# Kernel optimization log

Hardware: AMD Instinct MI355X
Metric: run time of the kernel (lower is better)

The kernel has to match this reference:

```python
import jax, jax.numpy as jnp
import numpy as np

BN_EPS = 1e-5


def setup_inputs() -> dict:
    key = jax.random.key(0)
    ks = jax.random.split(key, 8)
    B, C, H, W = 8, 256, 64, 64
    Ci = 128
    s_in = 1.0 / np.sqrt(C)
    s_int = 1.0 / np.sqrt(Ci)
    return {
        "x": jax.random.normal(ks[0], (B, C, H, W), jnp.float32),
        "w_g": jax.random.normal(ks[1], (Ci, C), jnp.float32) * s_in,
        "b_g": jnp.zeros((Ci,), jnp.float32),
        "w_theta": jax.random.normal(ks[2], (Ci, C), jnp.float32) * s_in,
        "b_theta": jnp.zeros((Ci,), jnp.float32),
        "w_phi": jax.random.normal(ks[3], (Ci, C), jnp.float32) * s_in,
        "b_phi": jnp.zeros((Ci,), jnp.float32),
        "w_out": jax.random.normal(ks[4], (C, Ci), jnp.float32) * s_int,
        "b_out": jnp.zeros((C,), jnp.float32),
        "bn_gamma": jnp.ones((C,), jnp.float32),
        "bn_beta": jnp.zeros((C,), jnp.float32),
        "bn_mean": jnp.zeros((C,), jnp.float32),
        "bn_var": jnp.ones((C,), jnp.float32),
    }


def reference(x, w_g, b_g, w_theta, b_theta, w_phi, b_phi, w_out, b_out,
              bn_gamma, bn_beta, bn_mean, bn_var):
    B, C, H, W = x.shape
    Ci = w_g.shape[0]
    N = H * W
    # 1x1 convs == per-pixel linear projections
    g = (jnp.einsum('bchw,oc->bhwo', x, w_g) + b_g).reshape(B, N, Ci)
    theta = (jnp.einsum('bchw,oc->bhwo', x, w_theta) + b_theta).reshape(B, N, Ci)
    phi = (jnp.einsum('bchw,oc->bohw', x, w_phi) + b_phi[:, None, None]).reshape(B, Ci, N)
    # full N x N attention (no scaling, as in the original)
    att = jax.nn.softmax(jnp.einsum('bnc,bcm->bnm', theta, phi), axis=-1)
    y = jnp.einsum('bnm,bmc->bnc', att, g).reshape(B, H, W, Ci)
    # output 1x1 conv + inference-mode BatchNorm (per-channel affine)
    out = jnp.einsum('bhwc,oc->bohw', y, w_out) + b_out[:, None, None]
    inv = bn_gamma / jnp.sqrt(bn_var + BN_EPS)
    out = out * inv[:, None, None] + (bn_beta - bn_mean * inv)[:, None, None]
    return x + out
```

## Files before the change

kernel.cpp:

```cpp
#include <hip/hip_runtime.h>
#include <math.h>

#define BB 8
#define CC 256
#define CI 128
#define NN 4096
#define BN_EPS 1e-5f
#define LOG2E 1.4426950408889634f
#define FIXMAX 88.0f

typedef unsigned int uint;
typedef unsigned short ushort;
typedef __bf16 bf16x8 __attribute__((ext_vector_type(8)));
typedef _Float16 f16x8 __attribute__((ext_vector_type(8)));
typedef float f32x16 __attribute__((ext_vector_type(16)));

__device__ __forceinline__ ushort bfbits(float f) {
    return __builtin_bit_cast(ushort, (__bf16)f);
}
__device__ __forceinline__ ushort hbits(float f) {
    return __builtin_bit_cast(ushort, (_Float16)f);
}
__device__ __forceinline__ float bf2f(ushort h) {
    return __uint_as_float(((uint)h) << 16);
}
__device__ __forceinline__ uint pk2(float a, float b) {
    return (uint)bfbits(a) | ((uint)bfbits(b) << 16);
}
__device__ __forceinline__ void gload16(const void* g, void* l) {
    __builtin_amdgcn_global_load_lds(
        (const __attribute__((address_space(1))) uint*)g,
        (__attribute__((address_space(3))) uint*)l, 16, 0, 0);
}
__device__ __forceinline__ bf16x8 asbf8(uint4 v) { return __builtin_bit_cast(bf16x8, v); }
__device__ __forceinline__ float fexp2(float a) {
    float e;
    asm("v_exp_f32 %0, %1" : "=v"(e) : "v"(a));
    return e;
}

__global__ __launch_bounds__(256) void wconv_kernel(
    const float* __restrict__ w_t, const float* __restrict__ w_p,
    const float* __restrict__ w_g, const float* __restrict__ w_o,
    const float* __restrict__ bn_g, const float* __restrict__ bn_b,
    const float* __restrict__ bn_m, const float* __restrict__ bn_v,
    const float* __restrict__ b_out,
    uint4* __restrict__ wt_h, uint4* __restrict__ wt_l,
    uint4* __restrict__ wp_h, uint4* __restrict__ wp_l,
    uint4* __restrict__ wg_h, uint4* __restrict__ wg_l,
    uint4* __restrict__ wo_h, uint4* __restrict__ wo_l,
    float* __restrict__ scale, float* __restrict__ shift)
{
    const int t = threadIdx.x, blk = blockIdx.x;
    if (blk == 64) {
        float inv = bn_g[t] * rsqrtf(bn_v[t] + BN_EPS);
        scale[t] = inv;
        shift[t] = b_out[t] * inv + bn_b[t] - bn_m[t] * inv;
        return;
    }
    int u = blk * 256 + t;
    int mat = u >> 12, ul = u & 4095;
    const float* src;
    uint4 *dh, *dl;
    int o, oct, C, O;
    if (mat == 0)      { src = w_t; dh = wt_h; dl = wt_l; }
    else if (mat == 1) { src = w_p; dh = wp_h; dl = wp_l; }
    else if (mat == 2) { src = w_g; dh = wg_h; dl = wg_l; }
    else               { src = w_o; dh = wo_h; dl = wo_l; }
    if (mat < 3) { O = 128; C = 256; o = ul >> 5; oct = ul & 31; }
    else         { O = 256; C = 128; o = ul >> 4; oct = ul & 15; }
    const float* s = src + (size_t)o * C + oct * 8;
    float4 va = *(const float4*)s, vb = *(const float4*)(s + 4);
    float v[8] = {va.x, va.y, va.z, va.w, vb.x, vb.y, vb.z, vb.w};
    uint hw[4], lw[4];
#pragma unroll
    for (int j = 0; j < 4; j++) {
        float a = v[2 * j], c = v[2 * j + 1];
        ushort ha = bfbits(a), hc = bfbits(c);
        hw[j] = (uint)ha | ((uint)hc << 16);
        lw[j] = pk2(a - bf2f(ha), c - bf2f(hc));
    }
    int di = oct * O + o;
    dh[di] = make_uint4(hw[0], hw[1], hw[2], hw[3]);
    dl[di] = make_uint4(lw[0], lw[1], lw[2], lw[3]);
}

__global__ __launch_bounds__(256, 2) void proj3_mfma(
    const float* __restrict__ x,
    const uint4* __restrict__ wt_h, const uint4* __restrict__ wt_l,
    const uint4* __restrict__ wp_h, const uint4* __restrict__ wp_l,
    const uint4* __restrict__ wg_h, const uint4* __restrict__ wg_l,
    const float* __restrict__ b_t, const float* __restrict__ b_p,
    const float* __restrict__ b_g,
    ushort* __restrict__ th, ushort* __restrict__ phi, ushort* __restrict__ gT)
{
    __shared__ __align__(16) char xsm[65536];
    const int t  = threadIdx.x;
    const int w  = t >> 6, l = t & 63;
    const int lq = l & 31, h = l >> 5;
    const int b  = blockIdx.x >> 6;
    const int n0 = (blockIdx.x & 63) << 6;

    {
        const int nq = t & 15;
#pragma unroll
        for (int i = 0; i < 2; i++) {
            int oct = (t >> 4) + 16 * i;
            const float* xp = x + ((size_t)b * CC + oct * 8) * NN + n0 + nq * 4;
            float4 r[8];
#pragma unroll
            for (int j = 0; j < 8; j++) r[j] = *(const float4*)(xp + (size_t)j * NN);
#pragma unroll
            for (int k = 0; k < 4; k++) {
                int n = nq * 4 + k;
                float v[8];
#pragma unroll
                for (int j = 0; j < 8; j++) v[j] = ((const float*)&r[j])[k];
                uint hw[4], lw[4];
#pragma unroll
                for (int j = 0; j < 4; j++) {
                    ushort ha = bfbits(v[2 * j]), hc = bfbits(v[2 * j + 1]);
                    hw[j] = (uint)ha | ((uint)hc << 16);
                    lw[j] = pk2(v[2 * j] - bf2f(ha), v[2 * j + 1] - bf2f(hc));
                }
                int uu = oct ^ (n & 31);
                *(uint4*)(xsm + n * 512 + uu * 16) = make_uint4(hw[0], hw[1], hw[2], hw[3]);
                *(uint4*)(xsm + 32768 + n * 512 + uu * 16) = make_uint4(lw[0], lw[1], lw[2], lw[3]);
            }
        }
    }
    __syncthreads();

    const int wo16 = w * 32 + lq;
    f32x16 acc[3][2];
    {
        float bt = b_t[wo16], bp = b_p[wo16];
        acc[0][0] = (f32x16)bt; acc[0][1] = (f32x16)bt;
        acc[1][0] = (f32x16)bp; acc[1][1] = (f32x16)bp;
        acc[2][0] = (f32x16)0.0f; acc[2][1] = (f32x16)0.0f;
    }

#pragma unroll 2
    for (int cs = 0; cs < 16; cs++) {
        int wi = (cs * 2 + h) * 128 + wo16;
        bf16x8 fth = asbf8(wt_h[wi]), ftl = asbf8(wt_l[wi]);
        bf16x8 fph = asbf8(wp_h[wi]), fpl = asbf8(wp_l[wi]);
        bf16x8 fgh = asbf8(wg_h[wi]), fgl = asbf8(wg_l[wi]);
        int xoff = lq * 512 + 16 * ((cs * 2 + h) ^ lq);
        bf16x8 xh0 = asbf8(*(const uint4*)(xsm + xoff));
        bf16x8 xh1 = asbf8(*(const uint4*)(xsm + 16384 + xoff));
        bf16x8 xl0 = asbf8(*(const uint4*)(xsm + 32768 + xoff));
        bf16x8 xl1 = asbf8(*(const uint4*)(xsm + 49152 + xoff));

        acc[0][0] = __builtin_amdgcn_mfma_f32_32x32x16_bf16(xh0, fth, acc[0][0], 0, 0, 0);
        acc[0][0] = __builtin_amdgcn_mfma_f32_32x32x16_bf16(xl0, fth, acc[0][0], 0, 0, 0);
        acc[0][0] = __builtin_amdgcn_mfma_f32_32x32x16_bf16(xh0, ftl, acc[0][0], 0, 0, 0);
        acc[0][1] = __builtin_amdgcn_mfma_f32_32x32x16_bf16(xh1, fth, acc[0][1], 0, 0, 0);
        acc[0][1] = __builtin_amdgcn_mfma_f32_32x32x16_bf16(xl1, fth, acc[0][1], 0, 0, 0);
        acc[0][1] = __builtin_amdgcn_mfma_f32_32x32x16_bf16(xh1, ftl, acc[0][1], 0, 0, 0);

        acc[1][0] = __builtin_amdgcn_mfma_f32_32x32x16_bf16(xh0, fph, acc[1][0], 0, 0, 0);
        acc[1][0] = __builtin_amdgcn_mfma_f32_32x32x16_bf16(xl0, fph, acc[1][0], 0, 0, 0);
        acc[1][0] = __builtin_amdgcn_mfma_f32_32x32x16_bf16(xh0, fpl, acc[1][0], 0, 0, 0);
        acc[1][1] = __builtin_amdgcn_mfma_f32_32x32x16_bf16(xh1, fph, acc[1][1], 0, 0, 0);
        acc[1][1] = __builtin_amdgcn_mfma_f32_32x32x16_bf16(xl1, fph, acc[1][1], 0, 0, 0);
        acc[1][1] = __builtin_amdgcn_mfma_f32_32x32x16_bf16(xh1, fpl, acc[1][1], 0, 0, 0);

        acc[2][0] = __builtin_amdgcn_mfma_f32_32x32x16_bf16(fgh, xh0, acc[2][0], 0, 0, 0);
        acc[2][0] = __builtin_amdgcn_mfma_f32_32x32x16_bf16(fgh, xl0, acc[2][0], 0, 0, 0);
        acc[2][0] = __builtin_amdgcn_mfma_f32_32x32x16_bf16(fgl, xh0, acc[2][0], 0, 0, 0);
        acc[2][1] = __builtin_amdgcn_mfma_f32_32x32x16_bf16(fgh, xh1, acc[2][1], 0, 0, 0);
        acc[2][1] = __builtin_amdgcn_mfma_f32_32x32x16_bf16(fgh, xl1, acc[2][1], 0, 0, 0);
        acc[2][1] = __builtin_amdgcn_mfma_f32_32x32x16_bf16(fgl, xh1, acc[2][1], 0, 0, 0);
    }

#pragma unroll
    for (int ns = 0; ns < 2; ns++) {
        size_t nb = (size_t)b * NN + n0 + ns * 32;
#pragma unroll
        for (int r = 0; r < 16; r++) {
            int nr = (r & 3) + 8 * (r >> 2) + 4 * h;
            size_t idx = (nb + nr) * CI + wo16;
            th[idx]  = hbits(acc[0][ns][r] * LOG2E);
            phi[idx] = hbits(acc[1][ns][r]);
        }
#pragma unroll
        for (int r = 0; r < 16; r++) {
            int orow = w * 32 + (r & 3) + 8 * (r >> 2) + 4 * h;
            gT[((size_t)b * CI + orow) * NN + n0 + ns * 32 + lq] =
                bfbits(acc[2][ns][r] + b_g[orow]);
        }
    }
}

__global__ __launch_bounds__(512, 2) void attn_mfma(
    const ushort* __restrict__ th, const ushort* __restrict__ phi,
    const ushort* __restrict__ gT,
    ushort* __restrict__ yh, ushort* __restrict__ yl)
{
    __shared__ __align__(16) char sm[131072];
    const int t    = threadIdx.x;
    const int w    = t >> 6, l = t & 63;
    const int wg   = w & 3, half = w >> 2;
    const int lq   = l & 31, h = l >> 5;
    const int b    = blockIdx.x & 7, qt = blockIdx.x >> 3;
    const int q0   = qt * 128 + wg * 32;

    f16x8 thf[8];
    {
        const char* thp = (const char*)(th + ((size_t)b * NN + q0 + lq) * CI);
#pragma unroll
        for (int cs = 0; cs < 8; cs++)
            thf[cs] = __builtin_bit_cast(f16x8, *(const uint4*)(thp + cs * 32 + h * 16));
    }

    const char* phig = (const char*)(phi + (size_t)b * NN * CI);
    const char* gTg  = (const char*)(gT + (size_t)b * NN * CI);
    char* smh = sm + half * 65536;

    f32x16 ya[4];
#pragma unroll
    for (int ct = 0; ct < 4; ct++) ya[ct] = (f32x16)0.0f;
    float l_run = 0.0f;

    auto stage = [&](int buf, int tile) {
        const char* ps = phig + (size_t)tile * 16384;
        const char* gs = gTg + (size_t)tile * 128;
        char* lb = smh + buf * 32768;
#pragma unroll
        for (int j = 0; j < 4; j++) {
            int c  = wg * 4 + j;
            int r  = c * 4 + (l >> 4);
            int cp = ((l & 15) * 16) ^ ((r & 15) << 4);
            gload16(ps + (size_t)r * 256 + cp, lb + c * 1024);
            int r8 = c * 8 + (l >> 3);
            int cg = ((l & 7) * 16) ^ ((r8 & 7) << 4);
            gload16(gs + (size_t)r8 * (NN * 2) + cg, lb + 16384 + c * 1024);
        }
    };

    stage(0, half * 32 + 0);
    stage(1, half * 32 + 1);
    asm volatile("s_waitcnt vmcnt(8)" ::: "memory");
    __builtin_amdgcn_s_barrier();
    __builtin_amdgcn_sched_barrier(0);

    const int swp = (lq & 15) << 4;
    const int swg = (lq & 7) << 4;

    for (int it = 0; it < 32; it++) {
        const char* smb = smh + (it & 1) * 32768;

        f32x16 sa0 = (f32x16)0.0f, sa1 = (f32x16)0.0f;
        __builtin_amdgcn_s_setprio(1);
#pragma unroll
        for (int cs = 0; cs < 8; cs++) {
            f16x8 f0 = __builtin_bit_cast(f16x8,
                *(const uint4*)(smb + lq * 256 + ((cs * 32 + h * 16) ^ swp)));
            f16x8 f1 = __builtin_bit_cast(f16x8,
                *(const uint4*)(smb + (32 + lq) * 256 + ((cs * 32 + h * 16) ^ swp)));
            sa0 = __builtin_amdgcn_mfma_f32_32x32x16_f16(f0, thf[cs], sa0, 0, 0, 0);
            sa1 = __builtin_amdgcn_mfma_f32_32x32x16_f16(f1, thf[cs], sa1, 0, 0, 0);
        }
        __builtin_amdgcn_s_setprio(0);

        {
            float t0 = 0.f, t1 = 0.f, t2 = 0.f, t3 = 0.f;
#pragma unroll
            for (int r = 0; r < 16; r += 4) {
                sa0[r]     = fexp2(sa0[r] - FIXMAX);     t0 += sa0[r];
                sa0[r + 1] = fexp2(sa0[r + 1] - FIXMAX); t1 += sa0[r + 1];
                sa0[r + 2] = fexp2(sa0[r + 2] - FIXMAX); t2 += sa0[r + 2];
                sa0[r + 3] = fexp2(sa0[r + 3] - FIXMAX); t3 += sa0[r + 3];
            }
#pragma unroll
            for (int r = 0; r < 16; r += 4) {
                sa1[r]     = fexp2(sa1[r] - FIXMAX);     t0 += sa1[r];
                sa1[r + 1] = fexp2(sa1[r + 1] - FIXMAX); t1 += sa1[r + 1];
                sa1[r + 2] = fexp2(sa1[r + 2] - FIXMAX); t2 += sa1[r + 2];
                sa1[r + 3] = fexp2(sa1[r + 3] - FIXMAX); t3 += sa1[r + 3];
            }
            l_run += (t0 + t1) + (t2 + t3);
        }

        __builtin_amdgcn_s_setprio(1);
#pragma unroll
        for (int mt = 0; mt < 2; mt++) {
            const f32x16& pa = mt ? sa1 : sa0;
#pragma unroll
            for (int s = 0; s < 2; s++) {
                const int base = s * 8;
                uint a0 = pk2(pa[base + 0], pa[base + 1]);
                uint a1 = pk2(pa[base + 2], pa[base + 3]);
                uint b0 = pk2(pa[base + 4], pa[base + 5]);
                uint b1 = pk2(pa[base + 6], pa[base + 7]);
                asm volatile("v_permlane32_swap_b32 %0, %1" : "+v"(a0), "+v"(b0));
                asm volatile("v_permlane32_swap_b32 %0, %1" : "+v"(a1), "+v"(b1));
                bf16x8 pf = __builtin_bit_cast(bf16x8, make_uint4(a0, a1, b0, b1));
                const int ks = mt * 2 + s;
#pragma unroll
                for (int ct = 0; ct < 4; ct++) {
                    bf16x8 gf = __builtin_bit_cast(bf16x8,
                        *(const uint4*)(smb + 16384 + (ct * 32 + lq) * 128 +
                                        ((ks * 32 + h * 16) ^ swg)));
                    ya[ct] = __builtin_amdgcn_mfma_f32_32x32x16_bf16(gf, pf, ya[ct], 0, 0, 0);
                }
            }
        }
        __builtin_amdgcn_s_setprio(0);

        asm volatile("" ::: "memory");
        __builtin_amdgcn_s_barrier();
        if (it < 30) {
            stage(it & 1, half * 32 + it + 2);
            asm volatile("s_waitcnt vmcnt(8)" ::: "memory");
            __builtin_amdgcn_s_barrier();
            __builtin_amdgcn_sched_barrier(0);
        } else if (it == 30) {
            asm volatile("s_waitcnt vmcnt(0)" ::: "memory");
            __builtin_amdgcn_s_barrier();
            __builtin_amdgcn_sched_barrier(0);
        }
    }

    if (w >= 4) {
        float* dst = (float*)(sm + wg * 16384 + l * 256);
#pragma unroll
        for (int ct = 0; ct < 4; ct++)
#pragma unroll
            for (int r4 = 0; r4 < 4; r4++) {
                int u = (ct * 4 + r4) ^ (l & 15);
                *(float4*)((char*)dst + u * 16) =
                    make_float4(ya[ct][r4 * 4 + 0], ya[ct][r4 * 4 + 1],
                                ya[ct][r4 * 4 + 2], ya[ct][r4 * 4 + 3]);
            }
        ((float*)(sm + 65536))[wg * 64 + l] = l_run;
    }
    __syncthreads();
    if (w < 4) {
        float lself = l_run + __shfl_xor(l_run, 32);
        const float* lBp = (const float*)(sm + 65536) + wg * 64;
        float ltot = lself + lBp[lq] + lBp[lq + 32];
        float inv = 1.0f / ltot;
        const char* src = (const char*)(sm + wg * 16384 + l * 256);
        const size_t qb = ((size_t)b * NN + q0 + lq) * CI;
#pragma unroll
        for (int ct = 0; ct < 4; ct++)
#pragma unroll
            for (int r4 = 0; r4 < 4; r4++) {
                int u = (ct * 4 + r4) ^ (l & 15);
                float4 vB = *(const float4*)(src + u * 16);
                float v0 = (ya[ct][r4 * 4 + 0] + vB.x) * inv;
                float v1 = (ya[ct][r4 * 4 + 1] + vB.y) * inv;
                float v2 = (ya[ct][r4 * 4 + 2] + vB.z) * inv;
                float v3 = (ya[ct][r4 * 4 + 3] + vB.w) * inv;
                ushort h0 = bfbits(v0), h1 = bfbits(v1), h2 = bfbits(v2), h3 = bfbits(v3);
                uint2 hw = make_uint2((uint)h0 | ((uint)h1 << 16),
                                      (uint)h2 | ((uint)h3 << 16));
                uint2 lw = make_uint2(pk2(v0 - bf2f(h0), v1 - bf2f(h1)),
                                      pk2(v2 - bf2f(h2), v3 - bf2f(h3)));
                int co = 32 * ct + 8 * r4 + 4 * h;
                *(uint2*)(yh + qb + co) = hw;
                *(uint2*)(yl + qb + co) = lw;
            }
    }
}

__global__ __launch_bounds__(256, 2) void outproj_mfma(
    const ushort* __restrict__ yh, const ushort* __restrict__ yl,
    const uint4* __restrict__ wo_h, const uint4* __restrict__ wo_l,
    const float* __restrict__ scale, const float* __restrict__ shift,
    const float* __restrict__ x, float* __restrict__ out)
{
    __shared__ __align__(16) char ysm[32768];
    const int t  = threadIdx.x;
    const int w  = t >> 6, l = t & 63;
    const int lq = l & 31, h = l >> 5;
    const int b  = blockIdx.x >> 6;
    const int n0 = (blockIdx.x & 63) << 6;

    {
#pragma unroll
        for (int j = 0; j < 4; j++) {
            int idx = w * 64 + j * 256 + l;
            int row = idx >> 4, u = idx & 15;
            size_t srow = ((size_t)b * NN + n0 + row) * CI;
            int cb = 16 * (u ^ (row & 15));
            gload16((const char*)yh + srow * 2 + cb, ysm + (w * 64 + j * 256) * 16);
            gload16((const char*)yl + srow * 2 + cb, ysm + 16384 + (w * 64 + j * 256) * 16);
        }
    }
    __syncthreads();

#pragma unroll
    for (int oi = 0; oi < 2; oi++) {
        const int ot = w + oi * 4;
        const int ob = ot * 32 + lq;
        f32x16 a0 = (f32x16)0.0f, a1 = (f32x16)0.0f;
#pragma unroll 2
        for (int cs = 0; cs < 8; cs++) {
            int wi = (cs * 2 + h) * 256 + ob;
            bf16x8 wfh = asbf8(wo_h[wi]), wfl = asbf8(wo_l[wi]);
            int xoff = lq * 256 + 16 * ((cs * 2 + h) ^ (lq & 15));
            bf16x8 y0h = asbf8(*(const uint4*)(ysm + xoff));
            bf16x8 y1h = asbf8(*(const uint4*)(ysm + 8192 + xoff));
            bf16x8 y0l = asbf8(*(const uint4*)(ysm + 16384 + xoff));
            bf16x8 y1l = asbf8(*(const uint4*)(ysm + 24576 + xoff));
            a0 = __builtin_amdgcn_mfma_f32_32x32x16_bf16(wfh, y0h, a0, 0, 0, 0);
            a0 = __builtin_amdgcn_mfma_f32_32x32x16_bf16(wfl, y0h, a0, 0, 0, 0);
            a0 = __builtin_amdgcn_mfma_f32_32x32x16_bf16(wfh, y0l, a0, 0, 0, 0);
            a1 = __builtin_amdgcn_mfma_f32_32x32x16_bf16(wfh, y1h, a1, 0, 0, 0);
            a1 = __builtin_amdgcn_mfma_f32_32x32x16_bf16(wfl, y1h, a1, 0, 0, 0);
            a1 = __builtin_amdgcn_mfma_f32_32x32x16_bf16(wfh, y1l, a1, 0, 0, 0);
        }
#pragma unroll
        for (int ns = 0; ns < 2; ns++) {
            const f32x16& av = ns ? a1 : a0;
#pragma unroll
            for (int r = 0; r < 16; r++) {
                int o = ot * 32 + (r & 3) + 8 * (r >> 2) + 4 * h;
                size_t ai = ((size_t)b * CC + o) * NN + n0 + ns * 32 + lq;
                out[ai] = av[r] * scale[o] + shift[o] + x[ai];
            }
        }
    }
}

extern "C" void kernel_launch(void* const* d_in, const int* in_sizes, int n_in,
                              void* d_out, int out_size, void* d_ws, size_t ws_size,
                              hipStream_t stream) {
    const float* x       = (const float*)d_in[0];
    const float* w_g     = (const float*)d_in[1];
    const float* b_g     = (const float*)d_in[2];
    const float* w_theta = (const float*)d_in[3];
    const float* b_theta = (const float*)d_in[4];
    const float* w_phi   = (const float*)d_in[5];
    const float* b_phi   = (const float*)d_in[6];
    const float* w_out   = (const float*)d_in[7];
    const float* b_out   = (const float*)d_in[8];
    const float* bn_g    = (const float*)d_in[9];
    const float* bn_b    = (const float*)d_in[10];
    const float* bn_m    = (const float*)d_in[11];
    const float* bn_v    = (const float*)d_in[12];
    float* out = (float*)d_out;

    const size_t arr = (size_t)BB * NN * CI;
    ushort* thw   = (ushort*)d_ws;
    ushort* phiw  = thw + arr;
    ushort* gTw   = phiw + arr;
    ushort* yhb   = gTw + arr;
    ushort* ylb   = yhb + arr;
    uint4*  wt_h  = (uint4*)(ylb + arr);
    uint4*  wt_l  = wt_h + 4096;
    uint4*  wp_h  = wt_l + 4096;
    uint4*  wp_l  = wp_h + 4096;
    uint4*  wg_h  = wp_l + 4096;
    uint4*  wg_l  = wg_h + 4096;
    uint4*  wo_h  = wg_l + 4096;
    uint4*  wo_l  = wo_h + 4096;
    float*  scl   = (float*)(wo_l + 4096);
    float*  shf   = scl + 256;

    wconv_kernel<<<65, 256, 0, stream>>>(
        w_theta, w_phi, w_g, w_out, bn_g, bn_b, bn_m, bn_v, b_out,
        wt_h, wt_l, wp_h, wp_l, wg_h, wg_l, wo_h, wo_l, scl, shf);
    proj3_mfma<<<BB * 64, 256, 0, stream>>>(
        x, wt_h, wt_l, wp_h, wp_l, wg_h, wg_l, b_theta, b_phi, b_g,
        thw, phiw, gTw);
    attn_mfma<<<256, 512, 0, stream>>>(thw, phiw, gTw, yhb, ylb);
    outproj_mfma<<<BB * 64, 256, 0, stream>>>(
        yhb, ylb, wo_h, wo_l, scl, shf, x, out);
}
```

Measured before the change: 140.7 us.

## Software-pipeline QK^T of the next tile with softmax and PV of the current tile

Splits staging into separate phi and gT double buffers. The QK^T MFMAs for tile it+1 are now issued before the exp/sum and PV work of tile it, so the VALU exponentials can overlap the matrix-core work. Wait counts are adjusted so each phi tile is resident one iteration earlier than its gT tile. This costs an extra pair of 16-wide accumulators per lane, which raises register pressure and could lower occupancy.

```diff
diff --git a/kernel.cpp b/kernel.cpp
--- a/kernel.cpp
+++ b/kernel.cpp
@@ -223,87 +223,105 @@
     for (int ct = 0; ct < 4; ct++) ya[ct] = (f32x16)0.0f;
     float l_run = 0.0f;
 
-    auto stage = [&](int buf, int tile) {
+    auto stage_phi = [&](int slot, int tile) {
         const char* ps = phig + (size_t)tile * 16384;
-        const char* gs = gTg + (size_t)tile * 128;
-        char* lb = smh + buf * 32768;
+        char* lb = smh + slot * 16384;
 #pragma unroll
         for (int j = 0; j < 4; j++) {
             int c  = wg * 4 + j;
             int r  = c * 4 + (l >> 4);
             int cp = ((l & 15) * 16) ^ ((r & 15) << 4);
             gload16(ps + (size_t)r * 256 + cp, lb + c * 1024);
+        }
+    };
+    auto stage_gt = [&](int slot, int tile) {
+        const char* gs = gTg + (size_t)tile * 128;
+        char* lb = smh + 32768 + slot * 16384;
+#pragma unroll
+        for (int j = 0; j < 4; j++) {
+            int c  = wg * 4 + j;
             int r8 = c * 8 + (l >> 3);
             int cg = ((l & 7) * 16) ^ ((r8 & 7) << 4);
-            gload16(gs + (size_t)r8 * (NN * 2) + cg, lb + 16384 + c * 1024);
+            gload16(gs + (size_t)r8 * (NN * 2) + cg, lb + c * 1024);
         }
     };
 
-    stage(0, half * 32 + 0);
-    stage(1, half * 32 + 1);
-    asm volatile("s_waitcnt vmcnt(8)" ::: "memory");
+    const int swp = (lq & 15) << 4;
+    const int swg = (lq & 7) << 4;
+
+    auto qk = [&](const char* pb, f32x16& d0, f32x16& d1) {
+#pragma unroll
+        for (int cs = 0; cs < 8; cs++) {
+            f16x8 f0 = __builtin_bit_cast(f16x8,
+                *(const uint4*)(pb + lq * 256 + ((cs * 32 + h * 16) ^ swp)));
+            f16x8 f1 = __builtin_bit_cast(f16x8,
+                *(const uint4*)(pb + (32 + lq) * 256 + ((cs * 32 + h * 16) ^ swp)));
+            d0 = __builtin_amdgcn_mfma_f32_32x32x16_f16(f0, thf[cs], d0, 0, 0, 0);
+            d1 = __builtin_amdgcn_mfma_f32_32x32x16_f16(f1, thf[cs], d1, 0, 0, 0);
+        }
+    };
+
+    const int t0 = half * 32;
+    stage_phi(0, t0 + 0);
+    stage_phi(1, t0 + 1);
+    stage_gt(0, t0 + 0);
+    stage_gt(1, t0 + 1);
+    asm volatile("s_waitcnt vmcnt(4)" ::: "memory");
     __builtin_amdgcn_s_barrier();
     __builtin_amdgcn_sched_barrier(0);
 
-    const int swp = (lq & 15) << 4;
-    const int swg = (lq & 7) << 4;
+    f32x16 sa0 = (f32x16)0.0f, sa1 = (f32x16)0.0f;
+    __builtin_amdgcn_s_setprio(1);
+    qk(smh, sa0, sa1);
+    __builtin_amdgcn_s_setprio(0);
 
     for (int it = 0; it < 32; it++) {
-        const char* smb = smh + (it & 1) * 32768;
-
-        f32x16 sa0 = (f32x16)0.0f, sa1 = (f32x16)0.0f;
+        f32x16 nx0 = (f32x16)0.0f, nx1 = (f32x16)0.0f;
         __builtin_amdgcn_s_setprio(1);
-#pragma unroll
-        for (int cs = 0; cs < 8; cs++) {
-            f16x8 f0 = __builtin_bit_cast(f16x8,
-                *(const uint4*)(smb + lq * 256 + ((cs * 32 + h * 16) ^ swp)));
-            f16x8 f1 = __builtin_bit_cast(f16x8,
-                *(const uint4*)(smb + (32 + lq) * 256 + ((cs * 32 + h * 16) ^ swp)));
-            sa0 = __builtin_amdgcn_mfma_f32_32x32x16_f16(f0, thf[cs], sa0, 0, 0, 0);
-            sa1 = __builtin_amdgcn_mfma_f32_32x32x16_f16(f1, thf[cs], sa1, 0, 0, 0);
-        }
-        __builtin_amdgcn_s_setprio(0);
+        if (it < 31) qk(smh + ((it + 1) & 1) * 16384, nx0, nx1);
 
         {
-            float t0 = 0.f, t1 = 0.f, t2 = 0.f, t3 = 0.f;
+            float t0s = 0.f, t1s = 0.f, t2s = 0.f, t3s = 0.f;
 #pragma unroll
             for (int r = 0; r < 16; r += 4) {
-                sa0[r]     = fexp2(sa0[r] - FIXMAX);     t0 += sa0[r];
-                sa0[r + 1] = fexp2(sa0[r + 1] - FIXMAX); t1 += sa0[r + 1];
-                sa0[r + 2] = fexp2(sa0[r + 2] - FIXMAX); t2 += sa0[r + 2];
-                sa0[r + 3] = fexp2(sa0[r + 3] - FIXMAX); t3 += sa0[r + 3];
+                sa0[r]     = fexp2(sa0[r] - FIXMAX);     t0s += sa0[r];
+                sa0[r + 1] = fexp2(sa0[r + 1] - FIXMAX); t1s += sa0[r + 1];
+                sa0[r + 2] = fexp2(sa0[r + 2] - FIXMAX); t2s += sa0[r + 2];
+                sa0[r + 3] = fexp2(sa0[r + 3] - FIXMAX); t3s += sa0[r + 3];
             }
 #pragma unroll
             for (int r = 0; r < 16; r += 4) {
-                sa1[r]     = fexp2(sa1[r] - FIXMAX);     t0 += sa1[r];
-                sa1[r + 1] = fexp2(sa1[r + 1] - FIXMAX); t1 += sa1[r + 1];
-                sa1[r + 2] = fexp2(sa1[r + 2] - FIXMAX); t2 += sa1[r + 2];
-                sa1[r + 3] = fexp2(sa1[r + 3] - FIXMAX); t3 += sa1[r + 3];
-            }
-            l_run += (t0 + t1) + (t2 + t3);
-        }
-
-        __builtin_amdgcn_s_setprio(1);
-#pragma unroll
-        for (int mt = 0; mt < 2; mt++) {
-            const f32x16& pa = mt ? sa1 : sa0;
-#pragma unroll
-            for (int s = 0; s < 2; s++) {
-                const int base = s * 8;
-                uint a0 = pk2(pa[base + 0], pa[base + 1]);
-                uint a1 = pk2(pa[base + 2], pa[base + 3]);
-                uint b0 = pk2(pa[base + 4], pa[base + 5]);
-                uint b1 = pk2(pa[base + 6], pa[base + 7]);
-                asm volatile("v_permlane32_swap_b32 %0, %1" : "+v"(a0), "+v"(b0));
-                asm volatile("v_permlane32_swap_b32 %0, %1" : "+v"(a1), "+v"(b1));
-                bf16x8 pf = __builtin_bit_cast(bf16x8, make_uint4(a0, a1, b0, b1));
-                const int ks = mt * 2 + s;
-#pragma unroll
-                for (int ct = 0; ct < 4; ct++) {
-                    bf16x8 gf = __builtin_bit_cast(bf16x8,
-                        *(const uint4*)(smb + 16384 + (ct * 32 + lq) * 128 +
-                                        ((ks * 32 + h * 16) ^ swg)));
-                    ya[ct] = __builtin_amdgcn_mfma_f32_32x32x16_bf16(gf, pf, ya[ct], 0, 0, 0);
+                sa1[r]     = fexp2(sa1[r] - FIXMAX);     t0s += sa1[r];
+                sa1[r + 1] = fexp2(sa1[r + 1] - FIXMAX); t1s += sa1[r + 1];
+                sa1[r + 2] = fexp2(sa1[r + 2] - FIXMAX); t2s += sa1[r + 2];
+                sa1[r + 3] = fexp2(sa1[r + 3] - FIXMAX); t3s += sa1[r + 3];
+            }
+            l_run += (t0s + t1s) + (t2s + t3s);
+        }
+
+        {
+            const char* gb = smh + 32768 + (it & 1) * 16384;
+#pragma unroll
+            for (int mt = 0; mt < 2; mt++) {
+                const f32x16& pa = mt ? sa1 : sa0;
+#pragma unroll
+                for (int s = 0; s < 2; s++) {
+                    const int base = s * 8;
+                    uint a0 = pk2(pa[base + 0], pa[base + 1]);
+                    uint a1 = pk2(pa[base + 2], pa[base + 3]);
+                    uint b0 = pk2(pa[base + 4], pa[base + 5]);
+                    uint b1 = pk2(pa[base + 6], pa[base + 7]);
+                    asm volatile("v_permlane32_swap_b32 %0, %1" : "+v"(a0), "+v"(b0));
+                    asm volatile("v_permlane32_swap_b32 %0, %1" : "+v"(a1), "+v"(b1));
+                    bf16x8 pf = __builtin_bit_cast(bf16x8, make_uint4(a0, a1, b0, b1));
+                    const int ks = mt * 2 + s;
+#pragma unroll
+                    for (int ct = 0; ct < 4; ct++) {
+                        bf16x8 gf = __builtin_bit_cast(bf16x8,
+                            *(const uint4*)(gb + (ct * 32 + lq) * 128 +
+                                            ((ks * 32 + h * 16) ^ swg)));
+                        ya[ct] = __builtin_amdgcn_mfma_f32_32x32x16_bf16(gf, pf, ya[ct], 0, 0, 0);
+                    }
                 }
             }
         }
@@ -311,9 +329,10 @@
 
         asm volatile("" ::: "memory");
         __builtin_amdgcn_s_barrier();
-        if (it < 30) {
-            stage(it & 1, half * 32 + it + 2);
-            asm volatile("s_waitcnt vmcnt(8)" ::: "memory");
+        if (it <= 29) {
+            stage_phi(it & 1, t0 + it + 2);
+            stage_gt(it & 1, t0 + it + 2);
+            asm volatile("s_waitcnt vmcnt(4)" ::: "memory");
             __builtin_amdgcn_s_barrier();
             __builtin_amdgcn_sched_barrier(0);
         } else if (it == 30) {
@@ -321,6 +340,7 @@
             __builtin_amdgcn_s_barrier();
             __builtin_amdgcn_sched_barrier(0);
         }
+        if (it < 31) { sa0 = nx0; sa1 = nx1; }
     }
 
     if (w >= 4) {
```

After: 143.8 us. 2.2% more time.

## Split attention key range across separate blocks and merge partials in new kernel

Applied to the files above, without the earlier changes.

The attention kernel no longer splits the key range across two halves of a 512-thread block reduced through shared memory. It now launches twice as many 256-thread blocks, each handling half the keys. Each block writes a normalized bf16 partial output and its row sum to global memory, and a new ymerge kernel combines the two partials into the hi/lo bf16 outputs. The aim is to halve LDS per block and raise occupancy and block count, at the cost of an extra launch, extra global traffic, and bf16 rounding of the partials before merging.

```diff
diff --git a/kernel.cpp b/kernel.cpp
--- a/kernel.cpp
+++ b/kernel.cpp
@@ -24,6 +24,8 @@
 __device__ __forceinline__ float bf2f(ushort h) {
     return __uint_as_float(((uint)h) << 16);
 }
+__device__ __forceinline__ float bflo(uint v) { return __uint_as_float(v << 16); }
+__device__ __forceinline__ float bfhi(uint v) { return __uint_as_float(v & 0xffff0000u); }
 __device__ __forceinline__ uint pk2(float a, float b) {
     return (uint)bfbits(a) | ((uint)bfbits(b) << 16);
 }
@@ -193,18 +195,19 @@
     }
 }
 
-__global__ __launch_bounds__(512, 2) void attn_mfma(
+__global__ __launch_bounds__(256, 2) void attn_mfma(
     const ushort* __restrict__ th, const ushort* __restrict__ phi,
     const ushort* __restrict__ gT,
-    ushort* __restrict__ yh, ushort* __restrict__ yl)
+    ushort* __restrict__ yP, float* __restrict__ lP)
 {
-    __shared__ __align__(16) char sm[131072];
-    const int t    = threadIdx.x;
-    const int w    = t >> 6, l = t & 63;
-    const int wg   = w & 3, half = w >> 2;
-    const int lq   = l & 31, h = l >> 5;
-    const int b    = blockIdx.x & 7, qt = blockIdx.x >> 3;
-    const int q0   = qt * 128 + wg * 32;
+    __shared__ __align__(16) char sm[65536];
+    const int t  = threadIdx.x;
+    const int w  = t >> 6, l = t & 63;
+    const int lq = l & 31, h = l >> 5;
+    const int b  = blockIdx.x & 7;
+    const int qt = (blockIdx.x >> 3) & 31;
+    const int kt = blockIdx.x >> 8;
+    const int q0 = qt * 128 + w * 32;
 
     f16x8 thf[8];
     {
@@ -216,7 +219,6 @@
 
     const char* phig = (const char*)(phi + (size_t)b * NN * CI);
     const char* gTg  = (const char*)(gT + (size_t)b * NN * CI);
-    char* smh = sm + half * 65536;
 
     f32x16 ya[4];
 #pragma unroll
@@ -226,10 +228,10 @@
     auto stage = [&](int buf, int tile) {
         const char* ps = phig + (size_t)tile * 16384;
         const char* gs = gTg + (size_t)tile * 128;
-        char* lb = smh + buf * 32768;
+        char* lb = sm + buf * 32768;
 #pragma unroll
         for (int j = 0; j < 4; j++) {
-            int c  = wg * 4 + j;
+            int c  = w * 4 + j;
             int r  = c * 4 + (l >> 4);
             int cp = ((l & 15) * 16) ^ ((r & 15) << 4);
             gload16(ps + (size_t)r * 256 + cp, lb + c * 1024);
@@ -239,8 +241,9 @@
         }
     };
 
-    stage(0, half * 32 + 0);
-    stage(1, half * 32 + 1);
+    const int t0 = kt * 32;
+    stage(0, t0 + 0);
+    stage(1, t0 + 1);
     asm volatile("s_waitcnt vmcnt(8)" ::: "memory");
     __builtin_amdgcn_s_barrier();
     __builtin_amdgcn_sched_barrier(0);
@@ -249,7 +252,7 @@
     const int swg = (lq & 7) << 4;
 
     for (int it = 0; it < 32; it++) {
-        const char* smb = smh + (it & 1) * 32768;
+        const char* smb = sm + (it & 1) * 32768;
 
         f32x16 sa0 = (f32x16)0.0f, sa1 = (f32x16)0.0f;
         __builtin_amdgcn_s_setprio(1);
@@ -265,22 +268,22 @@
         __builtin_amdgcn_s_setprio(0);
 
         {
-            float t0 = 0.f, t1 = 0.f, t2 = 0.f, t3 = 0.f;
+            float t0s = 0.f, t1s = 0.f, t2s = 0.f, t3s = 0.f;
 #pragma unroll
             for (int r = 0; r < 16; r += 4) {
-                sa0[r]     = fexp2(sa0[r] - FIXMAX);     t0 += sa0[r];
-                sa0[r + 1] = fexp2(sa0[r + 1] - FIXMAX); t1 += sa0[r + 1];
-                sa0[r + 2] = fexp2(sa0[r + 2] - FIXMAX); t2 += sa0[r + 2];
-                sa0[r + 3] = fexp2(sa0[r + 3] - FIXMAX); t3 += sa0[r + 3];
+                sa0[r]     = fexp2(sa0[r] - FIXMAX);     t0s += sa0[r];
+                sa0[r + 1] = fexp2(sa0[r + 1] - FIXMAX); t1s += sa0[r + 1];
+                sa0[r + 2] = fexp2(sa0[r + 2] - FIXMAX); t2s += sa0[r + 2];
+                sa0[r + 3] = fexp2(sa0[r + 3] - FIXMAX); t3s += sa0[r + 3];
             }
 #pragma unroll
             for (int r = 0; r < 16; r += 4) {
-                sa1[r]     = fexp2(sa1[r] - FIXMAX);     t0 += sa1[r];
-                sa1[r + 1] = fexp2(sa1[r + 1] - FIXMAX); t1 += sa1[r + 1];
-                sa1[r + 2] = fexp2(sa1[r + 2] - FIXMAX); t2 += sa1[r + 2];
-                sa1[r + 3] = fexp2(sa1[r + 3] - FIXMAX); t3 += sa1[r + 3];
+                sa1[r]     = fexp2(sa1[r] - FIXMAX);     t0s += sa1[r];
+                sa1[r + 1] = fexp2(sa1[r + 1] - FIXMAX); t1s += sa1[r + 1];
+                sa1[r + 2] = fexp2(sa1[r + 2] - FIXMAX); t2s += sa1[r + 2];
+                sa1[r + 3] = fexp2(sa1[r + 3] - FIXMAX); t3s += sa1[r + 3];
             }
-            l_run += (t0 + t1) + (t2 + t3);
+            l_run += (t0s + t1s) + (t2s + t3s);
         }
 
         __builtin_amdgcn_s_setprio(1);
@@ -312,7 +315,7 @@
         asm volatile("" ::: "memory");
         __builtin_amdgcn_s_barrier();
         if (it < 30) {
-            stage(it & 1, half * 32 + it + 2);
+            stage(it & 1, t0 + it + 2);
             asm volatile("s_waitcnt vmcnt(8)" ::: "memory");
             __builtin_amdgcn_s_barrier();
             __builtin_amdgcn_sched_barrier(0);
@@ -323,47 +326,54 @@
         }
     }
 
-    if (w >= 4) {
-        float* dst = (float*)(sm + wg * 16384 + l * 256);
-#pragma unroll
-        for (int ct = 0; ct < 4; ct++)
-#pragma unroll
-            for (int r4 = 0; r4 < 4; r4++) {
-                int u = (ct * 4 + r4) ^ (l & 15);
-                *(float4*)((char*)dst + u * 16) =
-                    make_float4(ya[ct][r4 * 4 + 0], ya[ct][r4 * 4 + 1],
-                                ya[ct][r4 * 4 + 2], ya[ct][r4 * 4 + 3]);
-            }
-        ((float*)(sm + 65536))[wg * 64 + l] = l_run;
-    }
-    __syncthreads();
-    if (w < 4) {
-        float lself = l_run + __shfl_xor(l_run, 32);
-        const float* lBp = (const float*)(sm + 65536) + wg * 64;
-        float ltot = lself + lBp[lq] + lBp[lq + 32];
-        float inv = 1.0f / ltot;
-        const char* src = (const char*)(sm + wg * 16384 + l * 256);
-        const size_t qb = ((size_t)b * NN + q0 + lq) * CI;
-#pragma unroll
-        for (int ct = 0; ct < 4; ct++)
-#pragma unroll
-            for (int r4 = 0; r4 < 4; r4++) {
-                int u = (ct * 4 + r4) ^ (l & 15);
-                float4 vB = *(const float4*)(src + u * 16);
-                float v0 = (ya[ct][r4 * 4 + 0] + vB.x) * inv;
-                float v1 = (ya[ct][r4 * 4 + 1] + vB.y) * inv;
-                float v2 = (ya[ct][r4 * 4 + 2] + vB.z) * inv;
-                float v3 = (ya[ct][r4 * 4 + 3] + vB.w) * inv;
-                ushort h0 = bfbits(v0), h1 = bfbits(v1), h2 = bfbits(v2), h3 = bfbits(v3);
-                uint2 hw = make_uint2((uint)h0 | ((uint)h1 << 16),
-                                      (uint)h2 | ((uint)h3 << 16));
-                uint2 lw = make_uint2(pk2(v0 - bf2f(h0), v1 - bf2f(h1)),
-                                      pk2(v2 - bf2f(h2), v3 - bf2f(h3)));
-                int co = 32 * ct + 8 * r4 + 4 * h;
-                *(uint2*)(yh + qb + co) = hw;
-                *(uint2*)(yl + qb + co) = lw;
-            }
-    }
+    float ltot = l_run + __shfl_xor(l_run, 32);
+    if (h == 0) lP[((size_t)kt * 8 + b) * NN + q0 + lq] = ltot;
+    float inv = 1.0f / ltot;
+
+    ushort* yp = yP + (size_t)kt * ((size_t)BB * NN * CI);
+    const size_t qb = ((size_t)b * NN + q0 + lq) * CI;
+#pragma unroll
+    for (int ct = 0; ct < 4; ct++)
+#pragma unroll
+        for (int r4 = 0; r4 < 4; r4++) {
+            uint2 hw = make_uint2(
+                pk2(ya[ct][r4 * 4 + 0] * inv, ya[ct][r4 * 4 + 1] * inv),
+                pk2(ya[ct][r4 * 4 + 2] * inv, ya[ct][r4 * 4 + 3] * inv));
+            int co = 32 * ct + 8 * r4 + 4 * h;
+            *(uint2*)(yp + qb + co) = hw;
+        }
+}
+
+__global__ __launch_bounds__(256) void ymerge_kernel(
+    const ushort* __restrict__ yP, const float* __restrict__ lP,
+    ushort* __restrict__ yh, ushort* __restrict__ yl)
+{
+    const size_t ARRL = (size_t)BB * NN;
+    size_t g = (size_t)blockIdx.x * 256 + threadIdx.x;
+    size_t row = g >> 4;
+    int u = (int)(g & 15);
+
+    float lA = lP[row], lB = lP[ARRL + row];
+    float s = 1.0f / (lA + lB);
+    float a = lA * s, c = lB * s;
+
+    const uint4* y4 = (const uint4*)yP;
+    uint4 va = y4[row * 16 + u];
+    uint4 vb = y4[(ARRL * CI / 8) + row * 16 + u];
+    const uint* pa = (const uint*)&va;
+    const uint* pb = (const uint*)&vb;
+
+    uint ho[4], lo[4];
+#pragma unroll
+    for (int j = 0; j < 4; j++) {
+        float v0 = a * bflo(pa[j]) + c * bflo(pb[j]);
+        float v1 = a * bfhi(pa[j]) + c * bfhi(pb[j]);
+        ushort h0 = bfbits(v0), h1 = bfbits(v1);
+        ho[j] = (uint)h0 | ((uint)h1 << 16);
+        lo[j] = pk2(v0 - bf2f(h0), v1 - bf2f(h1));
+    }
+    ((uint4*)yh)[row * 16 + u] = make_uint4(ho[0], ho[1], ho[2], ho[3]);
+    ((uint4*)yl)[row * 16 + u] = make_uint4(lo[0], lo[1], lo[2], lo[3]);
 }
 
 __global__ __launch_bounds__(256, 2) void outproj_mfma(
@@ -448,9 +458,8 @@
     ushort* thw   = (ushort*)d_ws;
     ushort* phiw  = thw + arr;
     ushort* gTw   = phiw + arr;
-    ushort* yhb   = gTw + arr;
-    ushort* ylb   = yhb + arr;
-    uint4*  wt_h  = (uint4*)(ylb + arr);
+    ushort* yPb   = gTw + arr;
+    uint4*  wt_h  = (uint4*)(yPb + 2 * arr);
     uint4*  wt_l  = wt_h + 4096;
     uint4*  wp_h  = wt_l + 4096;
     uint4*  wp_l  = wp_h + 4096;
@@ -460,6 +469,9 @@
     uint4*  wo_l  = wo_h + 4096;
     float*  scl   = (float*)(wo_l + 4096);
     float*  shf   = scl + 256;
+    float*  lPb   = shf + 256;
+    ushort* yhb   = thw;
+    ushort* ylb   = phiw;
 
     wconv_kernel<<<65, 256, 0, stream>>>(
         w_theta, w_phi, w_g, w_out, bn_g, bn_b, bn_m, bn_v, b_out,
@@ -467,7 +479,8 @@
     proj3_mfma<<<BB * 64, 256, 0, stream>>>(
         x, wt_h, wt_l, wp_h, wp_l, wg_h, wg_l, b_theta, b_phi, b_g,
         thw, phiw, gTw);
-    attn_mfma<<<256, 512, 0, stream>>>(thw, phiw, gTw, yhb, ylb);
+    attn_mfma<<<512, 256, 0, stream>>>(thw, phiw, gTw, yPb, lPb);
+    ymerge_kernel<<<2048, 256, 0, stream>>>(yPb, lPb, yhb, ylb);
     outproj_mfma<<<BB * 64, 256, 0, stream>>>(
         yhb, ylb, wo_h, wo_l, scl, shf, x, out);
 }
```

After: 144.4 us. 2.6% more time.
